# Kernel optimization log

Hardware: AMD Instinct MI355X
Metric: run time of the kernel (lower is better)

Reference implementation:

```python
import jax, jax.numpy as jnp
import numpy as np


def _fake_quant(x, bits, axis):
    """AQT-style abs-max symmetric fake quantization.

    IntNumerics(bits, preserve_zero=True, preserve_max_val=True, clip=True,
    round=True) with AbsMaxCalibration: bound = 2^(bits-1)-1,
    scale = absmax/bound (stop-gradient), q = round(clip(x/scale)),
    dequant = q*scale. Round uses straight-through estimator.
    """
    bound = float(2 ** (bits - 1) - 1)
    absmax = jax.lax.stop_gradient(
        jnp.max(jnp.abs(x), axis=axis, keepdims=True))
    scale = absmax / bound
    scale = jnp.where(scale == 0.0, jnp.ones_like(scale), scale)
    s = x / scale
    clipped = jnp.clip(s, -bound, bound)  # clip_gradient=True semantics
    rounded = clipped + jax.lax.stop_gradient(jnp.round(clipped) - clipped)
    return rounded * scale


def setup_inputs() -> dict:
    key = jax.random.key(0)
    k1, k2, k3 = jax.random.split(key, 3)
    B, S, D, F = 4, 2048, 4096, 4096
    x = jax.random.normal(k1, (B, S, D), dtype=jnp.float32)
    # lecun_normal over (in, out)
    kernel = jax.random.normal(k2, (D, F), dtype=jnp.float32) / np.sqrt(D)
    bias = jax.random.normal(k3, (F,), dtype=jnp.float32) * 0.01
    return {"x": x, "kernel": kernel, "bias": bias}


def reference(x, kernel, bias):
    # int8 fake-quant of activations: abs-max over contracting (last) axis
    xq = _fake_quant(x, bits=8, axis=-1)
    # int8 fake-quant of kernel: abs-max over contracting axis (0) -> per out-col
    kq = _fake_quant(kernel, bits=8, axis=0)
    # quantized dot_general: contract last axis of x with axis 0 of kernel
    y = jnp.einsum('bsd,df->bsf', xq, kq)
    # int16 fake-quant of bias (calibration_axes=-1 over the whole vector)
    bq16 = _fake_quant(bias, bits=16, axis=-1)
    y = y + bq16[None, None, :]
    # int8 output requant, per-row abs-max over feature axis
    out = _fake_quant(y, bits=8, axis=-1)
    return out
```

## Files before the change

kernel.cpp:

```cpp
#include <hip/hip_runtime.h>
#include <stdint.h>

typedef int int32x4 __attribute__((ext_vector_type(4)));

#define M_ROWS 8192
#define K_DIM  4096
#define N_DIM  4096

#define GPTR(p) ((const __attribute__((address_space(1))) unsigned int*)(p))
#define LPTR(p) ((__attribute__((address_space(3))) unsigned int*)(p))

__device__ __forceinline__ float block_absmax_256(float v, float* red) {
#pragma unroll
  for (int off = 32; off > 0; off >>= 1)
    v = fmaxf(v, __shfl_down(v, off, 64));
  const int w = threadIdx.x >> 6;
  if ((threadIdx.x & 63) == 0) red[w] = v;
  __syncthreads();
  return fmaxf(fmaxf(red[0], red[1]), fmaxf(red[2], red[3]));
}

__global__ void quant_x_kernel(const float* __restrict__ x,
                               int8_t* __restrict__ qx,
                               float* __restrict__ sx) {
  __shared__ float red[4];
  const int row = blockIdx.x;
  const int t = threadIdx.x;
  const float* xr = x + (size_t)row * K_DIM;
  float4 v[4];
  float m = 0.0f;
#pragma unroll
  for (int i = 0; i < 4; ++i) {
    v[i] = *(const float4*)(xr + t * 16 + i * 4);
    m = fmaxf(m, fmaxf(fmaxf(fabsf(v[i].x), fabsf(v[i].y)),
                       fmaxf(fabsf(v[i].z), fabsf(v[i].w))));
  }
  float amax = block_absmax_256(m, red);
  float scale = amax / 127.0f;
  if (scale == 0.0f) scale = 1.0f;
  if (t == 0) sx[row] = scale;
  int words[4];
#pragma unroll
  for (int i = 0; i < 4; ++i) {
    float a = fminf(fmaxf(v[i].x / scale, -127.0f), 127.0f);
    float b = fminf(fmaxf(v[i].y / scale, -127.0f), 127.0f);
    float c = fminf(fmaxf(v[i].z / scale, -127.0f), 127.0f);
    float d = fminf(fmaxf(v[i].w / scale, -127.0f), 127.0f);
    int qa = (int)rintf(a), qb = (int)rintf(b), qc = (int)rintf(c), qd = (int)rintf(d);
    words[i] = (qa & 255) | ((qb & 255) << 8) | ((qc & 255) << 16) | ((qd & 255) << 24);
  }
  *(int4*)(qx + (size_t)row * K_DIM + t * 16) =
      make_int4(words[0], words[1], words[2], words[3]);
}

__global__ void colmax_kernel(const float* __restrict__ k,
                              unsigned int* __restrict__ cm) {
  const int c = blockIdx.x * 256 + threadIdx.x;
  const int r0 = blockIdx.y * 128;
  float m = 0.0f;
  for (int i = 0; i < 128; ++i)
    m = fmaxf(m, fabsf(k[(size_t)(r0 + i) * N_DIM + c]));
  atomicMax(&cm[c], __float_as_uint(m));
}

__global__ void finalize_kernel(const float* __restrict__ cm,
                                float* __restrict__ sk,
                                const float* __restrict__ bias,
                                float* __restrict__ bq) {
  __shared__ float red[4];
  const int t = threadIdx.x;
  if (blockIdx.x < 16) {
    const int c = blockIdx.x * 256 + t;
    float s = cm[c] / 127.0f;
    if (s == 0.0f) s = 1.0f;
    sk[c] = s;
  } else {
    float4 v[4];
    float m = 0.0f;
#pragma unroll
    for (int i = 0; i < 4; ++i) {
      v[i] = *(const float4*)(bias + t * 16 + i * 4);
      m = fmaxf(m, fmaxf(fmaxf(fabsf(v[i].x), fabsf(v[i].y)),
                         fmaxf(fabsf(v[i].z), fabsf(v[i].w))));
    }
    float amax = block_absmax_256(m, red);
    float s = amax / 32767.0f;
    if (s == 0.0f) s = 1.0f;
#pragma unroll
    for (int i = 0; i < 4; ++i) {
      float4 o;
      o.x = rintf(fminf(fmaxf(v[i].x / s, -32767.0f), 32767.0f)) * s;
      o.y = rintf(fminf(fmaxf(v[i].y / s, -32767.0f), 32767.0f)) * s;
      o.z = rintf(fminf(fmaxf(v[i].z / s, -32767.0f), 32767.0f)) * s;
      o.w = rintf(fminf(fmaxf(v[i].w / s, -32767.0f), 32767.0f)) * s;
      *(float4*)(bq + t * 16 + i * 4) = o;
    }
  }
}

__global__ void quant_kT_kernel(const float* __restrict__ kern,
                                const float* __restrict__ cm,
                                int8_t* __restrict__ qkT) {
  __shared__ int8_t tile[64][80];
  const int t = threadIdx.x;
  const int c0 = blockIdx.x * 64;
  const int r0 = blockIdx.y * 64;
  const int colg = (t & 15) * 4;
  const int row = t >> 4;
  float s[4];
#pragma unroll
  for (int j = 0; j < 4; ++j) {
    float v = cm[c0 + colg + j] / 127.0f;
    s[j] = (v == 0.0f) ? 1.0f : v;
  }
#pragma unroll
  for (int i = 0; i < 4; ++i) {
    const int r = row + i * 16;
    float4 v = *(const float4*)&kern[(size_t)(r0 + r) * N_DIM + c0 + colg];
    tile[colg + 0][r] = (int8_t)rintf(fminf(fmaxf(v.x / s[0], -127.0f), 127.0f));
    tile[colg + 1][r] = (int8_t)rintf(fminf(fmaxf(v.y / s[1], -127.0f), 127.0f));
    tile[colg + 2][r] = (int8_t)rintf(fminf(fmaxf(v.z / s[2], -127.0f), 127.0f));
    tile[colg + 3][r] = (int8_t)rintf(fminf(fmaxf(v.w / s[3], -127.0f), 127.0f));
  }
  __syncthreads();
  const int f = t >> 2;
  const int seg = (t & 3) * 16;
  int4 w = *(const int4*)&tile[f][seg];
  *(int4*)(qkT + (size_t)(c0 + f) * K_DIM + r0 + seg) = w;
}

#define BM 128
#define BN 128
#define BK 128

__global__ void gemm_kernel(const int8_t* __restrict__ qx,
                            const int8_t* __restrict__ qkT,
                            const float* __restrict__ sx,
                            const float* __restrict__ sk,
                            const float* __restrict__ bq,
                            float* __restrict__ out) {
  __shared__ int32x4 AsV[1024];
  __shared__ int32x4 BsV[1024];
  char* As = (char*)AsV;
  char* Bs = (char*)BsV;

  const int t = threadIdx.x;
  const int w = t >> 6;
  const int l = t & 63;
  const int wm = w >> 1, wn = w & 1;
  const int rowBase = blockIdx.y * BM;
  const int colBase = blockIdx.x * BN;

  const int8_t* gA = qx  + (size_t)(rowBase + (l >> 3)) * K_DIM
                         + (((l & 7) ^ (l >> 3)) * 16);
  const int8_t* gB = qkT + (size_t)(colBase + (l >> 3)) * K_DIM
                         + (((l & 7) ^ (l >> 3)) * 16);

  int arow[4], brow[4], soff[2];
#pragma unroll
  for (int mt = 0; mt < 4; ++mt)
    arow[mt] = (wm * 64 + mt * 16 + (l & 15)) * 128;
#pragma unroll
  for (int nt = 0; nt < 4; ++nt)
    brow[nt] = (wn * 64 + nt * 16 + (l & 15)) * 128;
#pragma unroll
  for (int s = 0; s < 2; ++s)
    soff[s] = ((s * 4 + (l >> 4)) ^ (l & 7)) * 16;

  int32x4 zero = {0, 0, 0, 0};
  int32x4 acc[4][4];
#pragma unroll
  for (int mt = 0; mt < 4; ++mt)
#pragma unroll
    for (int nt = 0; nt < 4; ++nt) acc[mt][nt] = zero;

  for (int k0 = 0; k0 < K_DIM; k0 += BK) {
    __syncthreads();
#pragma unroll
    for (int j = 0; j < 4; ++j) {
      const int ca = j * 4 + w;
      __builtin_amdgcn_global_load_lds(
          GPTR(gA + (size_t)ca * 8 * K_DIM + k0),
          LPTR(As + ca * 1024), 16, 0, 0);
      __builtin_amdgcn_global_load_lds(
          GPTR(gB + (size_t)ca * 8 * K_DIM + k0),
          LPTR(Bs + ca * 1024), 16, 0, 0);
    }
    __syncthreads();

#pragma unroll
    for (int s = 0; s < 2; ++s) {
      int32x4 af[4], bf[4];
#pragma unroll
      for (int mt = 0; mt < 4; ++mt)
        af[mt] = *(const int32x4*)(As + arow[mt] + soff[s]);
#pragma unroll
      for (int nt = 0; nt < 4; ++nt)
        bf[nt] = *(const int32x4*)(Bs + brow[nt] + soff[s]);
#pragma unroll
      for (int mt = 0; mt < 4; ++mt)
#pragma unroll
        for (int nt = 0; nt < 4; ++nt)
          acc[mt][nt] = __builtin_amdgcn_mfma_i32_16x16x64_i8(
              af[mt], bf[nt], acc[mt][nt], 0, 0, 0);
    }
  }

  const int lr = (l >> 4) * 4;
  const int lc = l & 15;
#pragma unroll
  for (int mt = 0; mt < 4; ++mt) {
    const int r0 = rowBase + wm * 64 + mt * 16 + lr;
    float sxr[4];
#pragma unroll
    for (int r = 0; r < 4; ++r) sxr[r] = sx[r0 + r];
#pragma unroll
    for (int nt = 0; nt < 4; ++nt) {
      const int c = colBase + wn * 64 + nt * 16 + lc;
      const float skc = sk[c];
      const float bqc = bq[c];
#pragma unroll
      for (int r = 0; r < 4; ++r)
        out[(size_t)(r0 + r) * N_DIM + c] =
            (float)acc[mt][nt][r] * (sxr[r] * skc) + bqc;
    }
  }
}

__global__ void requant_kernel(float* __restrict__ y) {
  __shared__ float red[4];
  const int row = blockIdx.x;
  const int t = threadIdx.x;
  float* yr = y + (size_t)row * N_DIM;
  float4 v[4];
  float m = 0.0f;
#pragma unroll
  for (int i = 0; i < 4; ++i) {
    v[i] = *(const float4*)(yr + i * 1024 + t * 4);
    m = fmaxf(m, fmaxf(fmaxf(fabsf(v[i].x), fabsf(v[i].y)),
                       fmaxf(fabsf(v[i].z), fabsf(v[i].w))));
  }
  float amax = block_absmax_256(m, red);
  float s = amax / 127.0f;
  if (s == 0.0f) s = 1.0f;
#pragma unroll
  for (int i = 0; i < 4; ++i) {
    float4 o;
    o.x = rintf(fminf(fmaxf(v[i].x / s, -127.0f), 127.0f)) * s;
    o.y = rintf(fminf(fmaxf(v[i].y / s, -127.0f), 127.0f)) * s;
    o.z = rintf(fminf(fmaxf(v[i].z / s, -127.0f), 127.0f)) * s;
    o.w = rintf(fminf(fmaxf(v[i].w / s, -127.0f), 127.0f)) * s;
    *(float4*)(yr + i * 1024 + t * 4) = o;
  }
}

extern "C" void kernel_launch(void* const* d_in, const int* in_sizes, int n_in,
                              void* d_out, int out_size, void* d_ws, size_t ws_size,
                              hipStream_t stream) {
  (void)in_sizes; (void)n_in; (void)out_size; (void)ws_size;
  const float* x    = (const float*)d_in[0];
  const float* kern = (const float*)d_in[1];
  const float* bias = (const float*)d_in[2];
  float* out = (float*)d_out;

  char* w8 = (char*)d_ws;
  int8_t* qx  = (int8_t*)w8;
  int8_t* qkT = (int8_t*)(w8 + 33554432);
  float* sx   = (float*)(w8 + 50331648);
  float* cm   = (float*)(w8 + 50331648 + 32768);
  float* sk   = (float*)(w8 + 50331648 + 49152);
  float* bq   = (float*)(w8 + 50331648 + 65536);

  hipMemsetAsync(cm, 0, 4096 * sizeof(float), stream);
  quant_x_kernel<<<M_ROWS, 256, 0, stream>>>(x, qx, sx);
  colmax_kernel<<<dim3(16, 32), 256, 0, stream>>>(kern, (unsigned int*)cm);
  finalize_kernel<<<17, 256, 0, stream>>>(cm, sk, bias, bq);
  quant_kT_kernel<<<dim3(64, 64), 256, 0, stream>>>(kern, cm, qkT);
  gemm_kernel<<<dim3(N_DIM / BN, M_ROWS / BM), 256, 0, stream>>>(qx, qkT, sx, sk, bq, out);
  requant_kernel<<<M_ROWS, 256, 0, stream>>>(out);
}
```

Before: 471.7 us.

## Double-buffer GEMM A tiles in LDS, stream B from registers, enlarge M tile

The int8 GEMM now uses 256x128 tiles with BK=64. A tiles are double-buffered in LDS via async global_load_lds, while each wave prefetches its B fragments straight from global into registers one step ahead. This cuts barriers per k-step and overlaps loads with MFMA work, at the cost of more accumulator registers (launch bounds of 2 blocks per CU). The column absmax drops its atomics and memset in favour of partial maxima reduced in the finalize kernel, quant_kT reads the precomputed scales, and quant_x uses coalesced float4 strides.

```diff
diff --git a/kernel.cpp b/kernel.cpp
--- a/kernel.cpp
+++ b/kernel.cpp
@@ -26,12 +26,12 @@
   __shared__ float red[4];
   const int row = blockIdx.x;
   const int t = threadIdx.x;
-  const float* xr = x + (size_t)row * K_DIM;
+  const float4* xr = (const float4*)(x + (size_t)row * K_DIM);
   float4 v[4];
   float m = 0.0f;
 #pragma unroll
   for (int i = 0; i < 4; ++i) {
-    v[i] = *(const float4*)(xr + t * 16 + i * 4);
+    v[i] = xr[i * 256 + t];
     m = fmaxf(m, fmaxf(fmaxf(fabsf(v[i].x), fabsf(v[i].y)),
                        fmaxf(fabsf(v[i].z), fabsf(v[i].w))));
   }
@@ -39,7 +39,7 @@
   float scale = amax / 127.0f;
   if (scale == 0.0f) scale = 1.0f;
   if (t == 0) sx[row] = scale;
-  int words[4];
+  int* qw = (int*)(qx + (size_t)row * K_DIM);
 #pragma unroll
   for (int i = 0; i < 4; ++i) {
     float a = fminf(fmaxf(v[i].x / scale, -127.0f), 127.0f);
@@ -47,23 +47,22 @@
     float c = fminf(fmaxf(v[i].z / scale, -127.0f), 127.0f);
     float d = fminf(fmaxf(v[i].w / scale, -127.0f), 127.0f);
     int qa = (int)rintf(a), qb = (int)rintf(b), qc = (int)rintf(c), qd = (int)rintf(d);
-    words[i] = (qa & 255) | ((qb & 255) << 8) | ((qc & 255) << 16) | ((qd & 255) << 24);
-  }
-  *(int4*)(qx + (size_t)row * K_DIM + t * 16) =
-      make_int4(words[0], words[1], words[2], words[3]);
+    qw[i * 256 + t] =
+        (qa & 255) | ((qb & 255) << 8) | ((qc & 255) << 16) | ((qd & 255) << 24);
+  }
 }
 
 __global__ void colmax_kernel(const float* __restrict__ k,
-                              unsigned int* __restrict__ cm) {
+                              float* __restrict__ cmp) {
   const int c = blockIdx.x * 256 + threadIdx.x;
   const int r0 = blockIdx.y * 128;
   float m = 0.0f;
   for (int i = 0; i < 128; ++i)
     m = fmaxf(m, fabsf(k[(size_t)(r0 + i) * N_DIM + c]));
-  atomicMax(&cm[c], __float_as_uint(m));
-}
-
-__global__ void finalize_kernel(const float* __restrict__ cm,
+  cmp[(size_t)blockIdx.y * N_DIM + c] = m;
+}
+
+__global__ void finalize_kernel(const float* __restrict__ cmp,
                                 float* __restrict__ sk,
                                 const float* __restrict__ bias,
                                 float* __restrict__ bq) {
@@ -71,7 +70,10 @@
   const int t = threadIdx.x;
   if (blockIdx.x < 16) {
     const int c = blockIdx.x * 256 + t;
-    float s = cm[c] / 127.0f;
+    float m = 0.0f;
+#pragma unroll
+    for (int i = 0; i < 32; ++i) m = fmaxf(m, cmp[(size_t)i * N_DIM + c]);
+    float s = m / 127.0f;
     if (s == 0.0f) s = 1.0f;
     sk[c] = s;
   } else {
@@ -99,7 +101,7 @@
 }
 
 __global__ void quant_kT_kernel(const float* __restrict__ kern,
-                                const float* __restrict__ cm,
+                                const float* __restrict__ sk,
                                 int8_t* __restrict__ qkT) {
   __shared__ int8_t tile[64][80];
   const int t = threadIdx.x;
@@ -109,10 +111,7 @@
   const int row = t >> 4;
   float s[4];
 #pragma unroll
-  for (int j = 0; j < 4; ++j) {
-    float v = cm[c0 + colg + j] / 127.0f;
-    s[j] = (v == 0.0f) ? 1.0f : v;
-  }
+  for (int j = 0; j < 4; ++j) s[j] = sk[c0 + colg + j];
 #pragma unroll
   for (int i = 0; i < 4; ++i) {
     const int r = row + i * 16;
@@ -129,20 +128,19 @@
   *(int4*)(qkT + (size_t)(c0 + f) * K_DIM + r0 + seg) = w;
 }
 
-#define BM 128
+#define BM 256
 #define BN 128
-#define BK 128
-
-__global__ void gemm_kernel(const int8_t* __restrict__ qx,
-                            const int8_t* __restrict__ qkT,
-                            const float* __restrict__ sx,
-                            const float* __restrict__ sk,
-                            const float* __restrict__ bq,
-                            float* __restrict__ out) {
-  __shared__ int32x4 AsV[1024];
-  __shared__ int32x4 BsV[1024];
+#define BK 64
+
+__global__ __launch_bounds__(256, 2)
+void gemm_kernel(const int8_t* __restrict__ qx,
+                 const int8_t* __restrict__ qkT,
+                 const float* __restrict__ sx,
+                 const float* __restrict__ sk,
+                 const float* __restrict__ bq,
+                 float* __restrict__ out) {
+  __shared__ int32x4 AsV[2048];
   char* As = (char*)AsV;
-  char* Bs = (char*)BsV;
 
   const int t = threadIdx.x;
   const int w = t >> 6;
@@ -151,78 +149,99 @@
   const int rowBase = blockIdx.y * BM;
   const int colBase = blockIdx.x * BN;
 
-  const int8_t* gA = qx  + (size_t)(rowBase + (l >> 3)) * K_DIM
-                         + (((l & 7) ^ (l >> 3)) * 16);
-  const int8_t* gB = qkT + (size_t)(colBase + (l >> 3)) * K_DIM
-                         + (((l & 7) ^ (l >> 3)) * 16);
-
-  int arow[4], brow[4], soff[2];
-#pragma unroll
-  for (int mt = 0; mt < 4; ++mt)
-    arow[mt] = (wm * 64 + mt * 16 + (l & 15)) * 128;
+  const int8_t* gA = qx + (size_t)(rowBase + (t >> 2)) * K_DIM
+                        + (((t & 3) ^ ((t >> 2) & 3)) << 4);
+  const int8_t* gB = qkT + (size_t)(colBase + wn * 64 + (l & 15)) * K_DIM
+                         + ((l >> 4) << 4);
+
+  int aoff[8];
+#pragma unroll
+  for (int mt = 0; mt < 8; ++mt)
+    aoff[mt] = (wm * 128 + mt * 16 + (l & 15)) * 64 + (((l >> 4) ^ (l & 3)) << 4);
+
+  int32x4 zero = {0, 0, 0, 0};
+  int32x4 acc[8][4];
+#pragma unroll
+  for (int mt = 0; mt < 8; ++mt)
+#pragma unroll
+    for (int nt = 0; nt < 4; ++nt) acc[mt][nt] = zero;
+
+  int32x4 bc[4], bn[4];
+
+#pragma unroll
+  for (int j = 0; j < 4; ++j)
+    __builtin_amdgcn_global_load_lds(GPTR(gA + (size_t)j * 64 * K_DIM),
+                                     LPTR(As + j * 4096 + w * 1024), 16, 0, 0);
 #pragma unroll
   for (int nt = 0; nt < 4; ++nt)
-    brow[nt] = (wn * 64 + nt * 16 + (l & 15)) * 128;
-#pragma unroll
-  for (int s = 0; s < 2; ++s)
-    soff[s] = ((s * 4 + (l >> 4)) ^ (l & 7)) * 16;
-
-  int32x4 zero = {0, 0, 0, 0};
-  int32x4 acc[4][4];
-#pragma unroll
-  for (int mt = 0; mt < 4; ++mt)
-#pragma unroll
-    for (int nt = 0; nt < 4; ++nt) acc[mt][nt] = zero;
-
-  for (int k0 = 0; k0 < K_DIM; k0 += BK) {
+    bc[nt] = *(const int32x4*)(gB + (size_t)nt * 16 * K_DIM);
+  __syncthreads();
+
+  int buf = 0;
+  for (int i = 0; i < 63; ++i) {
+    const int kn = (i + 1) * BK;
+    char* dst = As + ((buf ^ 1) << 14) + w * 1024;
+#pragma unroll
+    for (int j = 0; j < 4; ++j)
+      __builtin_amdgcn_global_load_lds(GPTR(gA + (size_t)j * 64 * K_DIM + kn),
+                                       LPTR(dst + j * 4096), 16, 0, 0);
+#pragma unroll
+    for (int nt = 0; nt < 4; ++nt)
+      bn[nt] = *(const int32x4*)(gB + (size_t)nt * 16 * K_DIM + kn);
+
+    const char* Ab = As + (buf << 14);
+    int32x4 af[8];
+#pragma unroll
+    for (int mt = 0; mt < 8; ++mt)
+      af[mt] = *(const int32x4*)(Ab + aoff[mt]);
+#pragma unroll
+    for (int mt = 0; mt < 8; ++mt)
+#pragma unroll
+      for (int nt = 0; nt < 4; ++nt)
+        acc[mt][nt] = __builtin_amdgcn_mfma_i32_16x16x64_i8(
+            af[mt], bc[nt], acc[mt][nt], 0, 0, 0);
+
     __syncthreads();
 #pragma unroll
-    for (int j = 0; j < 4; ++j) {
-      const int ca = j * 4 + w;
-      __builtin_amdgcn_global_load_lds(
-          GPTR(gA + (size_t)ca * 8 * K_DIM + k0),
-          LPTR(As + ca * 1024), 16, 0, 0);
-      __builtin_amdgcn_global_load_lds(
-          GPTR(gB + (size_t)ca * 8 * K_DIM + k0),
-          LPTR(Bs + ca * 1024), 16, 0, 0);
-    }
-    __syncthreads();
-
-#pragma unroll
-    for (int s = 0; s < 2; ++s) {
-      int32x4 af[4], bf[4];
-#pragma unroll
-      for (int mt = 0; mt < 4; ++mt)
-        af[mt] = *(const int32x4*)(As + arow[mt] + soff[s]);
+    for (int nt = 0; nt < 4; ++nt) bc[nt] = bn[nt];
+    buf ^= 1;
+  }
+  {
+    const char* Ab = As + (buf << 14);
+    int32x4 af[8];
+#pragma unroll
+    for (int mt = 0; mt < 8; ++mt)
+      af[mt] = *(const int32x4*)(Ab + aoff[mt]);
+#pragma unroll
+    for (int mt = 0; mt < 8; ++mt)
 #pragma unroll
       for (int nt = 0; nt < 4; ++nt)
-        bf[nt] = *(const int32x4*)(Bs + brow[nt] + soff[s]);
-#pragma unroll
-      for (int mt = 0; mt < 4; ++mt)
-#pragma unroll
-        for (int nt = 0; nt < 4; ++nt)
-          acc[mt][nt] = __builtin_amdgcn_mfma_i32_16x16x64_i8(
-              af[mt], bf[nt], acc[mt][nt], 0, 0, 0);
-    }
+        acc[mt][nt] = __builtin_amdgcn_mfma_i32_16x16x64_i8(
+            af[mt], bc[nt], acc[mt][nt], 0, 0, 0);
   }
 
   const int lr = (l >> 4) * 4;
   const int lc = l & 15;
-#pragma unroll
-  for (int mt = 0; mt < 4; ++mt) {
-    const int r0 = rowBase + wm * 64 + mt * 16 + lr;
+  float skc[4], bqc[4];
+#pragma unroll
+  for (int nt = 0; nt < 4; ++nt) {
+    const int c = colBase + wn * 64 + nt * 16 + lc;
+    skc[nt] = sk[c];
+    bqc[nt] = bq[c];
+  }
+#pragma unroll
+  for (int mt = 0; mt < 8; ++mt) {
+    const int r0 = rowBase + wm * 128 + mt * 16 + lr;
     float sxr[4];
 #pragma unroll
     for (int r = 0; r < 4; ++r) sxr[r] = sx[r0 + r];
 #pragma unroll
     for (int nt = 0; nt < 4; ++nt) {
       const int c = colBase + wn * 64 + nt * 16 + lc;
-      const float skc = sk[c];
-      const float bqc = bq[c];
 #pragma unroll
       for (int r = 0; r < 4; ++r)
         out[(size_t)(r0 + r) * N_DIM + c] =
-            (float)acc[mt][nt][r] * (sxr[r] * skc) + bqc;
+            (float)acc[mt][nt][r] * (sxr[r] * skc[nt]) + bqc[nt];
     }
   }
 }
@@ -266,16 +285,15 @@
   char* w8 = (char*)d_ws;
   int8_t* qx  = (int8_t*)w8;
   int8_t* qkT = (int8_t*)(w8 + 33554432);
+  float* cmp  = (float*)(w8 + 33554432);
   float* sx   = (float*)(w8 + 50331648);
-  float* cm   = (float*)(w8 + 50331648 + 32768);
-  float* sk   = (float*)(w8 + 50331648 + 49152);
-  float* bq   = (float*)(w8 + 50331648 + 65536);
-
-  hipMemsetAsync(cm, 0, 4096 * sizeof(float), stream);
+  float* sk   = (float*)(w8 + 50331648 + 32768);
+  float* bq   = (float*)(w8 + 50331648 + 49152);
+
   quant_x_kernel<<<M_ROWS, 256, 0, stream>>>(x, qx, sx);
-  colmax_kernel<<<dim3(16, 32), 256, 0, stream>>>(kern, (unsigned int*)cm);
-  finalize_kernel<<<17, 256, 0, stream>>>(cm, sk, bias, bq);
-  quant_kT_kernel<<<dim3(64, 64), 256, 0, stream>>>(kern, cm, qkT);
+  colmax_kernel<<<dim3(16, 32), 256, 0, stream>>>(kern, cmp);
+  finalize_kernel<<<17, 256, 0, stream>>>(cmp, sk, bias, bq);
+  quant_kT_kernel<<<dim3(64, 64), 256, 0, stream>>>(kern, sk, qkT);
   gemm_kernel<<<dim3(N_DIM / BN, M_ROWS / BM), 256, 0, stream>>>(qx, qkT, sx, sk, bq, out);
   requant_kernel<<<M_ROWS, 256, 0, stream>>>(out);
 }
```

After: 519.6 us. 1.1x slower.
